# Kernel optimization log

Hardware: AMD Instinct MI355X
Metric: run time of the kernel (lower is better)

## Reference

```python
import jax, jax.numpy as jnp
import numpy as np

BS, TS, NA, OS = 32, 256, 16, 512
HID, D, W = 1024, 128, 8            # sw_hidden_dim, sw_input_dim, sw_window_size
OUT, DEC, NACT = 512, 512, 30       # sw_output_dim, sw_decoder_hidden_layer, n_actions


def setup_inputs() -> dict:
    key = jax.random.key(0)
    ks = jax.random.split(key, 12)
    p = lambda k, shape: jax.random.normal(k, shape, jnp.float32) * 0.02
    return {
        "inputs": jax.random.normal(ks[0], (BS, TS, NA, OS), jnp.float32),
        "hidden_state": jnp.zeros((BS, NA, (W - 1) * D), jnp.float32),
        "w1": p(ks[1], (OS, HID)),        "b1": jnp.zeros((HID,), jnp.float32),
        "w2": p(ks[2], (HID, D)),         "b2": jnp.zeros((D,), jnp.float32),
        "w3": p(ks[3], (W * D, OUT)),     "b3": jnp.zeros((OUT,), jnp.float32),
        "w4": p(ks[4], (OUT, DEC)),       "b4": jnp.zeros((DEC,), jnp.float32),
        "w5": p(ks[5], (DEC, NACT)),      "b5": jnp.zeros((NACT,), jnp.float32),
    }


def reference(inputs, hidden_state, w1, b1, w2, b2, w3, b3, w4, b4, w5, b5):
    bs, ts, na, _ = inputs.shape
    # encoder: two pointwise MLP layers over (bs, ts, na, *)
    x = jax.nn.relu(inputs @ w1 + b1)          # (bs, ts, na, HID)
    x = jax.nn.relu(x @ w2 + b2)               # (bs, ts, na, D)
    # build the full frame sequence: W-1 hidden frames followed by ts encoded frames
    hid_frames = hidden_state.reshape(bs, na, W - 1, D)
    seq = jnp.concatenate([hid_frames, jnp.transpose(x, (0, 2, 1, 3))], axis=2)  # (bs, na, ts+W-1, D)
    # sliding windows: window at step t = frames [t, t+W) — vectorized over all t
    wins = jnp.stack([seq[:, :, i:i + ts, :] for i in range(W)], axis=3)  # (bs, na, ts, W, D)
    wins = wins.reshape(bs, na, ts, W * D)
    h = jax.nn.relu(wins @ w3 + b3)            # (bs, na, ts, OUT)
    h = jnp.transpose(h, (0, 2, 1, 3))         # (bs, ts, na, OUT)
    h = jax.nn.relu(h @ w4 + b4)               # (bs, ts, na, DEC)
    q = h @ w5 + b5                            # (bs, ts, na, NACT)
    # final carried window: last W-1 frames of the sequence, flattened per agent
    window = seq[:, :, ts:, :].reshape(bs, na, (W - 1) * D)
    return (q, window)
```

## Files before the change

### kernel.cpp

```cpp
#include <hip/hip_runtime.h>
#include <hip/hip_bf16.h>
#include <hip/hip_fp8.h>


#define DEVI __device__ __forceinline__

typedef float f32x4 __attribute__((ext_vector_type(4)));
typedef short s16x8 __attribute__((ext_vector_type(8)));
typedef short s16x4 __attribute__((ext_vector_type(4)));
typedef long long i64;
typedef unsigned long long u64;

#define ROWS 131072
#define SEQ_T 263

#define W2P_OFF 524288
#define W5P_OFF 1441792

#define W3P8_BYTE_OFF 2916352
#define SEQ8_BYTE_OFF 3440640
#define W4P8_BYTE_OFF 20971520
#define BIG_BYTE_OFF 37388288

DEVI short f2bf(float f) {
  union { __hip_bfloat16 h; short s; } u;
  u.h = __float2bfloat16(f);
  return u.s;
}
DEVI float bf2f(short s) {
  union { float f; unsigned int u; } v;
  v.u = ((unsigned int)(unsigned short)s) << 16;
  return v.f;
}

DEVI unsigned int f2e4(float f) {
  union { __hip_fp8_e4m3 h; unsigned char c; } u;
  u.h = __hip_fp8_e4m3(f);
  return (unsigned int)u.c;
}

#if __has_builtin(__builtin_amdgcn_cvt_pk_fp8_f32)
DEVI unsigned int pk4e4(float a, float b, float c, float d) {
  int v = 0;
  v = __builtin_amdgcn_cvt_pk_fp8_f32(a, b, v, false);
  v = __builtin_amdgcn_cvt_pk_fp8_f32(c, d, v, true);
  return (unsigned int)v;
}
#else
DEVI unsigned int pk4e4(float a, float b, float c, float d) {
  return f2e4(a) | (f2e4(b) << 8) | (f2e4(c) << 16) | (f2e4(d) << 24);
}
#endif

DEVI f32x4 MFMA(s16x8 a, s16x8 b, f32x4 c) {
  return __builtin_amdgcn_mfma_f32_16x16x32_bf16(a, b, c, 0, 0, 0);
}
DEVI f32x4 MFMA8(i64 a, i64 b, f32x4 c) {
  return __builtin_amdgcn_mfma_f32_16x16x32_fp8_fp8(a, b, c, 0, 0, 0);
}

__global__ __launch_bounds__(256) void prep_kernel(
    const float* __restrict__ w1, const float* __restrict__ w2,
    const float* __restrict__ w3, const float* __restrict__ w4,
    const float* __restrict__ w5, const float* __restrict__ hid,
    short* __restrict__ wp, unsigned char* __restrict__ wp8,
    unsigned char* __restrict__ w3p8, unsigned char* __restrict__ w4p8,
    unsigned char* __restrict__ seq8)
{
  int t0 = blockIdx.x * 256 + threadIdx.x;
  if (t0 < 671744) {
    int idx = t0;
    const float* src; int sh, Nsrc, local; long dsto;
    if (idx < W2P_OFF)     { src = w1; sh = 4; Nsrc = 1024; local = idx;           dsto = idx; }
    else if (idx < 655360) { src = w2; sh = 5; Nsrc = 128;  local = idx - W2P_OFF; dsto = idx; }
    else                   { src = w5; sh = 4; Nsrc = 30;   local = idx - 655360;  dsto = W5P_OFF + (idx - 655360); }
    int j    = local & 7;
    int lane = (local >> 3) & 63;
    int rest = local >> 9;
    int k0   = rest & ((1 << sh) - 1);
    int n0   = rest >> sh;
    int k = (k0 << 5) + ((lane >> 4) << 3) + j;
    int n = (n0 << 4) + (lane & 15);
    float v = (n < Nsrc) ? src[k * Nsrc + n] : 0.f;
    wp[dsto] = f2bf(v);
  } else if (t0 < 851968) {
    int t = t0 - 671744;
    const float* src; int nkshift, Nsrc, dt; unsigned char* dst;
    if (t < 65536)       { src = w1; dt = t;          nkshift = 4; Nsrc = 1024; dst = wp8; }
    else if (t < 81920)  { src = w2; dt = t - 65536;  nkshift = 5; Nsrc = 128;  dst = wp8 + 524288; }
    else if (t < 147456) { src = w3; dt = t - 81920;  nkshift = 5; Nsrc = 512;  dst = w3p8; }
    else                 { src = w4; dt = t - 147456; nkshift = 4; Nsrc = 512;  dst = w4p8; }
    int lane = dt & 63;
    int rest = dt >> 6;
    int k0   = rest & ((1 << nkshift) - 1);
    int n0   = rest >> nkshift;
    int kb = (k0 << 5) + ((lane >> 4) << 3);
    int n  = (n0 << 4) + (lane & 15);
    float v[8];
    #pragma unroll
    for (int j = 0; j < 8; ++j) v[j] = src[(kb + j) * Nsrc + n];
    u64 pk = (u64)pk4e4(v[0], v[1], v[2], v[3])
           | ((u64)pk4e4(v[4], v[5], v[6], v[7]) << 32);
    *(u64*)(dst + (long)dt * 8) = pk;
  } else {
    int t = t0 - 851968;
    int j = t & 15;
    int r = t >> 4;
    int i = r % 7;
    int ba = r / 7;
    int s = j ^ i;
    const float* src = hid + (r << 7) + (j << 3);
    f32x4 a = *(const f32x4*)src;
    f32x4 b = *(const f32x4*)(src + 4);
    u64 pk = (u64)pk4e4(a[0], a[1], a[2], a[3])
           | ((u64)pk4e4(b[0], b[1], b[2], b[3]) << 32);
    *(u64*)(seq8 + (ba * SEQ_T + i) * 128 + s * 8) = pk;
  }
}

__global__ __launch_bounds__(512, 4) void enc_kernel(
    const float* __restrict__ inp, const unsigned char* __restrict__ w1p8,
    const float* __restrict__ b1, const unsigned char* __restrict__ w2p8,
    const float* __restrict__ b2, unsigned char* __restrict__ seq8)
{
  __shared__ unsigned char As8[32768] __attribute__((aligned(16)));
  __shared__ unsigned char h1q8[32768] __attribute__((aligned(16)));
  const int tid = threadIdx.x;
  const int lane = tid & 63, wv = tid >> 6;
  const int l15 = lane & 15, lg = lane >> 4;
  const int rb = blockIdx.x << 6;

  #pragma unroll
  for (int it = 0; it < 8; ++it) {
    int g = it * 512 + tid;
    int row = g >> 6, j = g & 63;
    const float* s = inp + (long)(rb + row) * 512 + j * 8;
    f32x4 v0 = *(const f32x4*)s;
    f32x4 v1 = *(const f32x4*)(s + 4);
    u64 pk = (u64)pk4e4(v0[0], v0[1], v0[2], v0[3])
           | ((u64)pk4e4(v1[0], v1[1], v1[2], v1[3]) << 32);
    *(u64*)(As8 + (j << 9) + ((row ^ (j & 15)) << 3)) = pk;
  }
  __syncthreads();

  f32x4 z = {0.f, 0.f, 0.f, 0.f};
  f32x4 acc2[4] = {z, z, z, z};

  for (int p = 0; p < 2; ++p) {
    f32x4 acc1[4][4];
    #pragma unroll
    for (int i = 0; i < 4; ++i)
      #pragma unroll
      for (int j = 0; j < 4; ++j) acc1[i][j] = z;

    const unsigned char* wB = w1p8 + (((p * 32 + wv * 4) * 16) << 9) + lane * 8;

    i64 Wc[4], Wn[4];
    #pragma unroll
    for (int ci = 0; ci < 4; ++ci) {
      Wc[ci] = *(const i64*)(wB + ((ci * 16 + 0) << 9));
      Wn[ci] = *(const i64*)(wB + ((ci * 16 + 1) << 9));
    }

    #pragma unroll 1
    for (int k0 = 0; k0 < 16; ++k0) {
      int kn2 = (k0 + 2) & 15;
      i64 Wn2[4];
      #pragma unroll
      for (int ci = 0; ci < 4; ++ci) Wn2[ci] = *(const i64*)(wB + ((ci * 16 + kn2) << 9));
      int k2 = k0 * 4 + lg;
      int c = k2 & 15;
      i64 Xc[4];
      #pragma unroll
      for (int mi = 0; mi < 4; ++mi)
        Xc[mi] = *(const i64*)(As8 + (k2 << 9) + (((mi * 16 + l15) ^ c) << 3));
      #pragma unroll
      for (int ci = 0; ci < 4; ++ci)
        #pragma unroll
        for (int mi = 0; mi < 4; ++mi)
          acc1[ci][mi] = MFMA8(Wc[ci], Xc[mi], acc1[ci][mi]);
      #pragma unroll
      for (int ci = 0; ci < 4; ++ci) { Wc[ci] = Wn[ci]; Wn[ci] = Wn2[ci]; }
    }
    __syncthreads();
    #pragma unroll
    for (int ci = 0; ci < 4; ++ci) {
      f32x4 bv = *(const f32x4*)(b1 + p * 512 + wv * 64 + ci * 16 + lg * 4);
      int k2c = wv * 8 + ci * 2 + (lg >> 1);
      int half = (lg & 1) << 2;
      #pragma unroll
      for (int mi = 0; mi < 4; ++mi) {
        int m = mi * 16 + l15;
        unsigned int pk = pk4e4(fmaxf(acc1[ci][mi][0] + bv[0], 0.f),
                                fmaxf(acc1[ci][mi][1] + bv[1], 0.f),
                                fmaxf(acc1[ci][mi][2] + bv[2], 0.f),
                                fmaxf(acc1[ci][mi][3] + bv[3], 0.f));
        *(unsigned int*)(h1q8 + (k2c << 9) + (m << 3) + half) = pk;
      }
    }
    __syncthreads();
    const unsigned char* w2B = w2p8 + ((wv * 32 + p * 16) << 9) + lane * 8;
    i64 W2c = *(const i64*)(w2B);
    i64 W2n = *(const i64*)(w2B + (1 << 9));
    #pragma unroll 1
    for (int kk = 0; kk < 16; ++kk) {
      int kn2 = (kk + 2) & 15;
      i64 W2n2 = *(const i64*)(w2B + (kn2 << 9));
      i64 X2[4];
      #pragma unroll
      for (int mi = 0; mi < 4; ++mi)
        X2[mi] = *(const i64*)(h1q8 + ((kk * 4 + lg) << 9) + ((mi * 16 + l15) << 3));
      #pragma unroll
      for (int mi = 0; mi < 4; ++mi)
        acc2[mi] = MFMA8(W2c, X2[mi], acc2[mi]);
      W2c = W2n; W2n = W2n2;
    }
  }
  __syncthreads();
  unsigned char* scr8 = As8;
  {
    f32x4 bv = *(const f32x4*)(b2 + wv * 16 + lg * 4);
    int gsb = wv * 2 + (lg >> 1);
    int off4 = (lg & 1) << 2;
    #pragma unroll
    for (int mi = 0; mi < 4; ++mi) {
      int m = mi * 16 + l15;
      int f15 = ((rb >> 4) + mi + 7) & 15;
      unsigned int pk = pk4e4(fmaxf(acc2[mi][0] + bv[0], 0.f),
                              fmaxf(acc2[mi][1] + bv[1], 0.f),
                              fmaxf(acc2[mi][2] + bv[2], 0.f),
                              fmaxf(acc2[mi][3] + bv[3], 0.f));
      int ls = (gsb ^ f15) ^ (m & 15);
      *(unsigned int*)(scr8 + m * 128 + ls * 8 + off4) = pk;
    }
  }
  __syncthreads();
  #pragma unroll
  for (int it = 0; it < 2; ++it) {
    int c = it * 512 + tid;
    int i = c >> 4, s = c & 15;
    u64 v = *(const u64*)(scr8 + i * 128 + ((s ^ (i & 15)) << 3));
    int r = rb + i;
    int ba2 = ((r >> 12) << 4) + (r & 15);
    int t = (r >> 4) & 255;
    int f = t + 7;
    *(u64*)(seq8 + (ba2 * SEQ_T + f) * 128 + (s << 3)) = v;
  }
}

__global__ __launch_bounds__(256) void enc_hi_kernel(
    const float* __restrict__ inp, const short* __restrict__ w1p,
    const float* __restrict__ b1, const short* __restrict__ w2p,
    const float* __restrict__ b2, float* __restrict__ out)
{
  __shared__ short As[8192]  __attribute__((aligned(16)));
  __shared__ short h1s[16384] __attribute__((aligned(16)));
  const int tid = threadIdx.x;
  const int lane = tid & 63, wv = tid >> 6;
  const int l15 = lane & 15, lg = lane >> 4;
  const int b = blockIdx.x / 7, ti = blockIdx.x % 7;
  const int t = 249 + ti;
  const long row0 = (long)b * 4096 + t * 16;

  #pragma unroll
  for (int it = 0; it < 4; ++it) {
    int c = it * 256 + tid;
    int m = c >> 6, j = c & 63;
    const float* s = inp + (row0 + m) * 512 + j * 8;
    f32x4 v0 = *(const f32x4*)s;
    f32x4 v1 = *(const f32x4*)(s + 4);
    s16x8 o;
    o[0]=f2bf(v0[0]); o[1]=f2bf(v0[1]); o[2]=f2bf(v0[2]); o[3]=f2bf(v0[3]);
    o[4]=f2bf(v1[0]); o[5]=f2bf(v1[1]); o[6]=f2bf(v1[2]); o[7]=f2bf(v1[3]);
    *(s16x8*)((char*)As + (j << 8) + (((m ^ (j & 15)) & 15) << 4)) = o;
  }
  __syncthreads();

  f32x4 z = {0.f, 0.f, 0.f, 0.f};
  f32x4 acc1[16];
  #pragma unroll
  for (int i = 0; i < 16; ++i) acc1[i] = z;
  #pragma unroll 1
  for (int k0 = 0; k0 < 16; ++k0) {
    int k2 = k0 * 4 + lg;
    s16x8 X = *(const s16x8*)((const char*)As + (k2 << 8) + (((l15 ^ (k2 & 15)) & 15) << 4));
    #pragma unroll
    for (int ci = 0; ci < 16; ++ci) {
      s16x8 W = *(const s16x8*)(w1p + (((wv * 16 + ci) * 16 + k0) << 9) + lane * 8);
      acc1[ci] = MFMA(W, X, acc1[ci]);
    }
  }
  #pragma unroll
  for (int ci = 0; ci < 16; ++ci) {
    f32x4 bv = *(const f32x4*)(b1 + wv * 256 + ci * 16 + lg * 4);
    int k2c = wv * 32 + ci * 2 + (lg >> 1);
    int half = (lg & 1) << 3;
    s16x4 o;
    #pragma unroll
    for (int j = 0; j < 4; ++j)
      o[j] = f2bf(fmaxf(acc1[ci][j] + bv[j], 0.f));
    *(s16x4*)((char*)h1s + (k2c << 8) + (l15 << 4) + half) = o;
  }
  __syncthreads();
  f32x4 acc2[2] = {z, z};
  #pragma unroll 1
  for (int kk = 0; kk < 32; ++kk) {
    s16x8 X2 = *(const s16x8*)((const char*)h1s + ((kk * 4 + lg) << 8) + (l15 << 4));
    #pragma unroll
    for (int nf = 0; nf < 2; ++nf) {
      s16x8 W2 = *(const s16x8*)(w2p + (((wv * 2 + nf) * 32 + kk) << 9) + lane * 8);
      acc2[nf] = MFMA(W2, X2, acc2[nf]);
    }
  }
  #pragma unroll
  for (int nf = 0; nf < 2; ++nf) {
    #pragma unroll
    for (int rr = 0; rr < 4; ++rr) {
      int d = (wv * 2 + nf) * 16 + lg * 4 + rr;
      float v = fmaxf(acc2[nf][rr] + b2[d], 0.f);
      out[3932160 + (((b * 16 + l15) * 7 + ti) << 7) + d] = v;
    }
  }
}

__global__ __launch_bounds__(512, 4) void win_kernel(
    const unsigned char* __restrict__ seq8, const unsigned char* __restrict__ w3p8,
    const float* __restrict__ b3, unsigned char* __restrict__ h3p8)
{
  __shared__ unsigned char sh8[17280] __attribute__((aligned(16)));
  __shared__ short rp[8192] __attribute__((aligned(16)));
  const int tid = threadIdx.x;
  const int lane = tid & 63, wid = tid >> 6;
  const int wm = wid >> 2, wn = wid & 3;
  const int l15 = lane & 15, lg = lane >> 4;
  const int bid = blockIdx.x;
  const int th = bid & 1, ba = bid >> 1;
  const int t0 = th << 7;

  const unsigned char* gsrc = seq8 + (ba * SEQ_T + t0) * 128;
  #pragma unroll
  for (int i = 0; i < 3; ++i) {
    int c = i * 512 + tid;
    if (c < 1080) *(s16x8*)&sh8[c * 16] = *(const s16x8*)(gsrc + c * 16);
  }
  __syncthreads();

  f32x4 z = {0.f, 0.f, 0.f, 0.f};
  for (int h = 0; h < 2; ++h) {
    f32x4 acc[4][4];
    #pragma unroll
    for (int i = 0; i < 4; ++i)
      #pragma unroll
      for (int j = 0; j < 4; ++j) acc[i][j] = z;

    const unsigned char* bB = w3p8 + (((h * 16 + wn * 4) * 32) << 9) + lane * 8;
    i64 bcur[4];
    #pragma unroll
    for (int nf = 0; nf < 4; ++nf) bcur[nf] = *(const i64*)(bB + ((nf * 32) << 9));

    #pragma unroll 1
    for (int kc = 0; kc < 32; ++kc) {
      int kn = (kc + 1) & 31;
      i64 bnxt[4];
      #pragma unroll
      for (int nf = 0; nf < 4; ++nf) bnxt[nf] = *(const i64*)(bB + ((nf * 32 + kn) << 9));
      int w = kc >> 2;
      int dslot = ((kc & 3) << 2) + lg;
      i64 av[4];
      #pragma unroll
      for (int mf = 0; mf < 4; ++mf) {
        int f = wm * 64 + mf * 16 + l15 + w;
        av[mf] = *(const i64*)(sh8 + f * 128 + ((dslot ^ (f & 15)) << 3));
      }
      #pragma unroll
      for (int nf = 0; nf < 4; ++nf)
        #pragma unroll
        for (int mf = 0; mf < 4; ++mf)
          acc[mf][nf] = MFMA8(av[mf], bcur[nf], acc[mf][nf]);
      #pragma unroll
      for (int nf = 0; nf < 4; ++nf) bcur[nf] = bnxt[nf];
    }

    for (int s = 0; s < 4; ++s) {
      __syncthreads();
      #pragma unroll
      for (int mf = 0; mf < 4; ++mf) {
        float bias = b3[h * 256 + wn * 64 + s * 16 + l15];
        int lc = wn * 16 + l15;
        #pragma unroll
        for (int rr = 0; rr < 4; ++rr) {
          int row = wm * 64 + mf * 16 + lg * 4 + rr;
          float v = fmaxf(acc[mf][s][rr] + bias, 0.f);
          int by = ((row << 7) + (lc << 1)) ^ ((row & 7) << 4);
          rp[by >> 1] = f2bf(v);
        }
      }
      __syncthreads();
      #pragma unroll
      for (int it = 0; it < 2; ++it) {
        int c = it * 512 + tid;
        int cl = c & 15, qh = (c >> 4) & 1, wnl = (c >> 5) & 3, tt = (c >> 7) & 7;
        int row = tt * 16 + cl;
        int qb = wnl * 16 + qh * 8;
        int by = ((row << 7) + (qb << 1)) ^ ((row & 7) << 4);
        s16x8 v = *(const s16x8*)((const char*)rp + by);
        u64 pk = (u64)pk4e4(bf2f(v[0]), bf2f(v[1]), bf2f(v[2]), bf2f(v[3]))
               | ((u64)pk4e4(bf2f(v[4]), bf2f(v[5]), bf2f(v[6]), bf2f(v[7])) << 32);
        int k0g = h * 8 + wnl * 2 + (s >> 1);
        int g = ((s & 1) << 1) + qh;
        int mt = ba * 16 + th * 8 + tt;
        long dst = ((long)((mt * 16 + k0g) * 64 + g * 16 + cl)) << 3;
        *(u64*)(h3p8 + dst) = pk;
      }
    }
  }
}

__global__ __launch_bounds__(512, 4) void dec_kernel(
    const unsigned char* __restrict__ h3p8, const unsigned char* __restrict__ w4p8,
    const float* __restrict__ b4, const short* __restrict__ w5p,
    const float* __restrict__ b5, float* __restrict__ out)
{
  __shared__ short h4s[32768] __attribute__((aligned(16)));
  const int tid = threadIdx.x;
  const int lane = tid & 63, wid = tid >> 6;
  const int wm = wid >> 2, wn = wid & 3;
  const int mf5 = wid;
  const int l15 = lane & 15, lg = lane >> 4;
  const int rb = blockIdx.x << 7;

  f32x4 z = {0.f, 0.f, 0.f, 0.f};
  f32x4 acc5[2] = {z, z};
  const unsigned char* aBase = h3p8 + (long)((rb >> 4) + wm * 4) * 8192 + lane * 8;

  for (int h = 0; h < 2; ++h) {
    f32x4 acc[4][4];
    #pragma unroll
    for (int i = 0; i < 4; ++i)
      #pragma unroll
      for (int j = 0; j < 4; ++j) acc[i][j] = z;

    const unsigned char* bB = w4p8 + (((h * 16 + wn * 4) * 16) << 9) + lane * 8;
    i64 bcur[4];
    #pragma unroll
    for (int nf = 0; nf < 4; ++nf) bcur[nf] = *(const i64*)(bB + ((nf * 16) << 9));

    #pragma unroll 1
    for (int k0 = 0; k0 < 16; ++k0) {
      int kn = (k0 + 1) & 15;
      i64 bnxt[4];
      #pragma unroll
      for (int nf = 0; nf < 4; ++nf) bnxt[nf] = *(const i64*)(bB + ((nf * 16 + kn) << 9));
      i64 av[4];
      #pragma unroll
      for (int mf = 0; mf < 4; ++mf) av[mf] = *(const i64*)(aBase + mf * 8192 + k0 * 512);
      #pragma unroll
      for (int nf = 0; nf < 4; ++nf)
        #pragma unroll
        for (int mf = 0; mf < 4; ++mf)
          acc[mf][nf] = MFMA8(av[mf], bcur[nf], acc[mf][nf]);
      #pragma unroll
      for (int nf = 0; nf < 4; ++nf) bcur[nf] = bnxt[nf];
    }
    __syncthreads();
    #pragma unroll
    for (int mf = 0; mf < 4; ++mf)
      #pragma unroll
      for (int nf = 0; nf < 4; ++nf) {
        int lc = wn * 64 + nf * 16 + l15;
        float bias = b4[h * 256 + lc];
        #pragma unroll
        for (int rr = 0; rr < 4; ++rr) {
          int row = wm * 64 + mf * 16 + lg * 4 + rr;
          float v = fmaxf(acc[mf][nf][rr] + bias, 0.f);
          int by = ((row << 9) + (lc << 1)) ^ ((row & 7) << 4);
          h4s[by >> 1] = f2bf(v);
        }
      }
    __syncthreads();
    #pragma unroll
    for (int kk = 0; kk < 8; ++kk) {
      int row = mf5 * 16 + l15;
      int by = ((row << 9) + (kk << 6) + (lg << 4)) ^ ((row & 7) << 4);
      s16x8 a0 = *(const s16x8*)((const char*)h4s + by);
      #pragma unroll
      for (int nf = 0; nf < 2; ++nf) {
        s16x8 wb = *(const s16x8*)(w5p + (nf * 16 + h * 8 + kk) * 512 + lane * 8);
        acc5[nf] = MFMA(a0, wb, acc5[nf]);
      }
    }
  }
  #pragma unroll
  for (int nf = 0; nf < 2; ++nf) {
    int col = nf * 16 + l15;
    if (col < 30) {
      float bias = b5[col];
      #pragma unroll
      for (int rr = 0; rr < 4; ++rr) {
        int row_ = rb + mf5 * 16 + lg * 4 + rr;
        int t = row_ & 255;
        int ba2 = row_ >> 8;
        int orow = (((ba2 >> 4) << 8) + t) * 16 + (ba2 & 15);
        out[orow * 30 + col] = acc5[nf][rr] + bias;
      }
    }
  }
}

extern "C" void kernel_launch(void* const* d_in, const int* in_sizes, int n_in,
                              void* d_out, int out_size, void* d_ws, size_t ws_size,
                              hipStream_t stream) {
  const float* inp = (const float*)d_in[0];
  const float* hid = (const float*)d_in[1];
  const float* w1  = (const float*)d_in[2];
  const float* b1  = (const float*)d_in[3];
  const float* w2  = (const float*)d_in[4];
  const float* b2  = (const float*)d_in[5];
  const float* w3  = (const float*)d_in[6];
  const float* b3  = (const float*)d_in[7];
  const float* w4  = (const float*)d_in[8];
  const float* b4  = (const float*)d_in[9];
  const float* w5  = (const float*)d_in[10];
  const float* b5  = (const float*)d_in[11];

  char* ws = (char*)d_ws;
  short* wp   = (short*)ws;
  short* w1p  = wp;
  short* w2p  = wp + W2P_OFF;
  short* w5p  = wp + W5P_OFF;
  unsigned char* w3p8 = (unsigned char*)(ws + W3P8_BYTE_OFF);
  unsigned char* seq8 = (unsigned char*)(ws + SEQ8_BYTE_OFF);
  unsigned char* w4p8 = (unsigned char*)(ws + W4P8_BYTE_OFF);
  unsigned char* h3p8 = (unsigned char*)(ws + BIG_BYTE_OFF);
  unsigned char* w1p8 = h3p8;
  unsigned char* w2p8 = w1p8 + 524288;
  float* out  = (float*)d_out;

  prep_kernel   <<<3552, 256, 0, stream>>>(w1, w2, w3, w4, w5, hid,
                                           wp, w1p8, w3p8, w4p8, seq8);
  enc_kernel    <<<2048, 512, 0, stream>>>(inp, w1p8, b1, w2p8, b2, seq8);
  enc_hi_kernel <<<224, 256, 0, stream>>>(inp, w1p, b1, w2p, b2, out);
  win_kernel    <<<1024, 512, 0, stream>>>(seq8, w3p8, b3, h3p8);
  dec_kernel    <<<1024, 512, 0, stream>>>(h3p8, w4p8, b4, w5p, b5, out);
}
```

Before: 388.0 us.

## Split fused encoder into two kernels with FP8 hidden activations in global memory

The fused encoder kernel is split into enc1, which computes layer 1 and writes the FP8 hidden activations to a global scratch buffer, and enc2, which reloads a 64KB tile per block and runs layer 2 over the full K=1024. This removes the per-half LDS handoff and two block barriers from the fused kernel and cuts enc1's shared memory to 32KB, which may allow more blocks per CU. In exchange it adds a 128MB round trip of intermediate activations through global memory, an extra launch, and a 64KB LDS footprint in enc2. The w1p8/w2p8 weights move to a new workspace offset so they no longer alias the h1 scratch buffer.

```diff
diff --git a/kernel.cpp b/kernel.cpp
--- a/kernel.cpp
+++ b/kernel.cpp
@@ -20,6 +20,7 @@
 #define W3P8_BYTE_OFF 2916352
 #define SEQ8_BYTE_OFF 3440640
 #define W4P8_BYTE_OFF 20971520
+#define W12P8_BYTE_OFF 21233664
 #define BIG_BYTE_OFF 37388288
 
 DEVI short f2bf(float f) {
@@ -118,13 +119,11 @@
   }
 }
 
-__global__ __launch_bounds__(512, 4) void enc_kernel(
+__global__ __launch_bounds__(512, 4) void enc1_kernel(
     const float* __restrict__ inp, const unsigned char* __restrict__ w1p8,
-    const float* __restrict__ b1, const unsigned char* __restrict__ w2p8,
-    const float* __restrict__ b2, unsigned char* __restrict__ seq8)
+    const float* __restrict__ b1, unsigned char* __restrict__ h1g)
 {
   __shared__ unsigned char As8[32768] __attribute__((aligned(16)));
-  __shared__ unsigned char h1q8[32768] __attribute__((aligned(16)));
   const int tid = threadIdx.x;
   const int lane = tid & 63, wv = tid >> 6;
   const int l15 = lane & 15, lg = lane >> 4;
@@ -144,7 +143,7 @@
   __syncthreads();
 
   f32x4 z = {0.f, 0.f, 0.f, 0.f};
-  f32x4 acc2[4] = {z, z, z, z};
+  unsigned char* hb = h1g + ((long)blockIdx.x << 16);
 
   for (int p = 0; p < 2; ++p) {
     f32x4 acc1[4][4];
@@ -182,11 +181,10 @@
       #pragma unroll
       for (int ci = 0; ci < 4; ++ci) { Wc[ci] = Wn[ci]; Wn[ci] = Wn2[ci]; }
     }
-    __syncthreads();
     #pragma unroll
     for (int ci = 0; ci < 4; ++ci) {
       f32x4 bv = *(const f32x4*)(b1 + p * 512 + wv * 64 + ci * 16 + lg * 4);
-      int k2c = wv * 8 + ci * 2 + (lg >> 1);
+      int k2g = p * 64 + wv * 8 + ci * 2 + (lg >> 1);
       int half = (lg & 1) << 2;
       #pragma unroll
       for (int mi = 0; mi < 4; ++mi) {
@@ -195,29 +193,51 @@
                                 fmaxf(acc1[ci][mi][1] + bv[1], 0.f),
                                 fmaxf(acc1[ci][mi][2] + bv[2], 0.f),
                                 fmaxf(acc1[ci][mi][3] + bv[3], 0.f));
-        *(unsigned int*)(h1q8 + (k2c << 9) + (m << 3) + half) = pk;
-      }
-    }
-    __syncthreads();
-    const unsigned char* w2B = w2p8 + ((wv * 32 + p * 16) << 9) + lane * 8;
-    i64 W2c = *(const i64*)(w2B);
-    i64 W2n = *(const i64*)(w2B + (1 << 9));
-    #pragma unroll 1
-    for (int kk = 0; kk < 16; ++kk) {
-      int kn2 = (kk + 2) & 15;
-      i64 W2n2 = *(const i64*)(w2B + (kn2 << 9));
-      i64 X2[4];
-      #pragma unroll
-      for (int mi = 0; mi < 4; ++mi)
-        X2[mi] = *(const i64*)(h1q8 + ((kk * 4 + lg) << 9) + ((mi * 16 + l15) << 3));
-      #pragma unroll
-      for (int mi = 0; mi < 4; ++mi)
-        acc2[mi] = MFMA8(W2c, X2[mi], acc2[mi]);
-      W2c = W2n; W2n = W2n2;
-    }
-  }
-  __syncthreads();
-  unsigned char* scr8 = As8;
+        *(unsigned int*)(hb + (k2g << 9) + (m << 3) + half) = pk;
+      }
+    }
+  }
+}
+
+__global__ __launch_bounds__(512, 4) void enc2_kernel(
+    const unsigned char* __restrict__ h1g, const unsigned char* __restrict__ w2p8,
+    const float* __restrict__ b2, unsigned char* __restrict__ seq8)
+{
+  __shared__ unsigned char h1s8[65536] __attribute__((aligned(16)));
+  const int tid = threadIdx.x;
+  const int lane = tid & 63, wv = tid >> 6;
+  const int l15 = lane & 15, lg = lane >> 4;
+  const int rb = blockIdx.x << 6;
+
+  const unsigned char* src = h1g + ((long)blockIdx.x << 16);
+  #pragma unroll
+  for (int it = 0; it < 8; ++it) {
+    int c = it * 512 + tid;
+    *(s16x8*)(h1s8 + c * 16) = *(const s16x8*)(src + c * 16);
+  }
+  __syncthreads();
+
+  f32x4 z = {0.f, 0.f, 0.f, 0.f};
+  f32x4 acc2[4] = {z, z, z, z};
+
+  const unsigned char* w2B = w2p8 + ((wv * 32) << 9) + lane * 8;
+  i64 W2c = *(const i64*)(w2B);
+  i64 W2n = *(const i64*)(w2B + (1 << 9));
+  #pragma unroll 1
+  for (int kk = 0; kk < 32; ++kk) {
+    int kn2 = (kk + 2) & 31;
+    i64 W2n2 = *(const i64*)(w2B + (kn2 << 9));
+    i64 X2[4];
+    #pragma unroll
+    for (int mi = 0; mi < 4; ++mi)
+      X2[mi] = *(const i64*)(h1s8 + ((kk * 4 + lg) << 9) + ((mi * 16 + l15) << 3));
+    #pragma unroll
+    for (int mi = 0; mi < 4; ++mi)
+      acc2[mi] = MFMA8(W2c, X2[mi], acc2[mi]);
+    W2c = W2n; W2n = W2n2;
+  }
+  __syncthreads();
+  unsigned char* scr8 = h1s8;
   {
     f32x4 bv = *(const f32x4*)(b2 + wv * 16 + lg * 4);
     int gsb = wv * 2 + (lg >> 1);
@@ -531,14 +551,16 @@
   unsigned char* w3p8 = (unsigned char*)(ws + W3P8_BYTE_OFF);
   unsigned char* seq8 = (unsigned char*)(ws + SEQ8_BYTE_OFF);
   unsigned char* w4p8 = (unsigned char*)(ws + W4P8_BYTE_OFF);
+  unsigned char* w1p8 = (unsigned char*)(ws + W12P8_BYTE_OFF);
+  unsigned char* w2p8 = w1p8 + 524288;
+  unsigned char* h1g  = (unsigned char*)(ws + BIG_BYTE_OFF);
   unsigned char* h3p8 = (unsigned char*)(ws + BIG_BYTE_OFF);
-  unsigned char* w1p8 = h3p8;
-  unsigned char* w2p8 = w1p8 + 524288;
   float* out  = (float*)d_out;
 
   prep_kernel   <<<3552, 256, 0, stream>>>(w1, w2, w3, w4, w5, hid,
                                            wp, w1p8, w3p8, w4p8, seq8);
-  enc_kernel    <<<2048, 512, 0, stream>>>(inp, w1p8, b1, w2p8, b2, seq8);
+  enc1_kernel   <<<2048, 512, 0, stream>>>(inp, w1p8, b1, h1g);
+  enc2_kernel   <<<2048, 512, 0, stream>>>(h1g, w2p8, b2, seq8);
   enc_hi_kernel <<<224, 256, 0, stream>>>(inp, w1p, b1, w2p, b2, out);
   win_kernel    <<<1024, 512, 0, stream>>>(seq8, w3p8, b3, h3p8);
   dec_kernel    <<<1024, 512, 0, stream>>>(h3p8, w4p8, b4, w5p, b5, out);
```

New measurement: 443.8 us. +14.4%, slower.
